# Kernel optimization log

Hardware: AMD Instinct MI355X
Metric: run time of the kernel (lower is better)

Reference implementation:

```python
import jax, jax.numpy as jnp
import numpy as np

DECAY = 0.99
EPS = 1e-05


def setup_inputs() -> dict:
    key = jax.random.key(0)
    k1, k2, k3 = jax.random.split(key, 3)
    x = jax.random.normal(k1, (16, 4096, 512), dtype=jnp.float32)
    embed = jax.random.normal(k2, (1024, 512), dtype=jnp.float32)
    cluster_size = jnp.ones((1024,), dtype=jnp.float32)
    embed_avg = jax.random.normal(k3, (1024, 512), dtype=jnp.float32)
    return {"x": x, "embed": embed, "cluster_size": cluster_size, "embed_avg": embed_avg}


def reference(x, embed, cluster_size, embed_avg):
    # x: [..., d]; embed: [K, d]
    K, d = embed.shape
    xf = x.reshape(-1, d)  # [N, d]
    dist = -(jnp.sum(xf * xf, axis=1, keepdims=True)
             - 2.0 * (xf @ embed.T)
             + jnp.sum(embed * embed, axis=1)[None, :])  # [N, K]
    ind = jnp.argmax(dist, axis=-1)  # [N]
    quantize = embed[ind].reshape(x.shape)  # dequantize (embedding lookup)
    embed_ind = ind.reshape(x.shape[:-1])
    # Training-mode EMA updates (one-hot scatter expressed as segment adds)
    counts = jnp.zeros((K,), dtype=x.dtype).at[ind].add(1.0)           # onehot.sum(0)
    embed_sum = jnp.zeros((K, d), dtype=x.dtype).at[ind].add(xf)       # (x^T @ onehot)^T
    new_cluster_size = cluster_size * DECAY + (1.0 - DECAY) * counts
    new_embed_avg = embed_avg * DECAY + (1.0 - DECAY) * embed_sum
    n = jnp.sum(new_cluster_size)
    cs = (new_cluster_size + EPS) / (n + K * EPS) * n  # laplace smoothing * total
    new_embed = new_embed_avg / cs[:, None]
    return (quantize, embed_ind, new_cluster_size, new_embed_avg, new_embed)
```

## Files before the change

kernel.cpp:

```cpp
#include <hip/hip_runtime.h>

typedef unsigned short ushort_t;
typedef __attribute__((ext_vector_type(8))) short bf16x8;
typedef __attribute__((ext_vector_type(4))) float f32x4;

#define DECAY 0.99f
#define EPS 1e-5f
#define K_CODES 1024
#define D 512
#define N_ROWS 65536
#define MARGIN 0.0625f

#define BM 128
#define NKT 8
#define NCH 16

#define CHUNK 64
#define MAX_CHUNKS 2048

#define XH_OFF   0u
#define XL_OFF   67108864u
#define EH_OFF   134217728u
#define EL_OFF   135266304u
#define ESUM_OFF 136314880u
#define CNT_OFF  138412032u
#define E2_OFF   138416128u
#define NFLAG_OFF 138420224u
#define NPTR_OFF  138420228u
#define FLAGS_OFF 138420480u
#define WS_NEED  (138420480u + 262144u)
#define ROWLIST_OFF   0u
#define BASE_OFF      262144u
#define CURSOR_OFF    266240u
#define CHUNKBASE_OFF 270336u
#define DESC_OFF      274432u
#define PARTIAL_OFF   307200u

__device__ inline ushort_t f2bf(float f) {
    unsigned int u = __float_as_uint(f);
    unsigned int r = (u + 0x7FFFu + ((u >> 16) & 1u)) >> 16;
    return (ushort_t)r;
}
__device__ inline float bf2f(ushort_t h) { return __uint_as_float(((unsigned int)h) << 16); }

__device__ inline void gload16_lds(const void* g, void* l) {
    __builtin_amdgcn_global_load_lds(
        (const __attribute__((address_space(1))) unsigned int*)g,
        (__attribute__((address_space(3))) unsigned int*)l, 16, 0, 0);
}

__global__ __launch_bounds__(256) void prep_split(const float* __restrict__ src,
                                                  ushort_t* __restrict__ hi,
                                                  ushort_t* __restrict__ lo) {
    const int g = blockIdx.x * 256 + threadIdx.x;
    const int ln = g & 63;
    const int tc = g >> 6;
    const int C = tc & 15;
    const int R = tc >> 4;
    const int row = (R << 4) + (ln & 15);
    const int k = (C << 5) + ((ln >> 4) << 3);
    const float4 v0 = *(const float4*)(src + (size_t)row * D + k);
    const float4 v1 = *(const float4*)(src + (size_t)row * D + k + 4);
    float v[8] = {v0.x, v0.y, v0.z, v0.w, v1.x, v1.y, v1.z, v1.w};
    short h[8], l[8];
    #pragma unroll
    for (int i = 0; i < 8; ++i) {
        ushort_t hh = f2bf(v[i]);
        h[i] = (short)hh;
        l[i] = (short)f2bf(v[i] - bf2f(hh));
    }
    bf16x8 hv = {h[0], h[1], h[2], h[3], h[4], h[5], h[6], h[7]};
    bf16x8 lv = {l[0], l[1], l[2], l[3], l[4], l[5], l[6], l[7]};
    *(bf16x8*)(hi + (size_t)g * 8) = hv;
    *(bf16x8*)(lo + (size_t)g * 8) = lv;
}

__global__ __launch_bounds__(64) void e2_kernel(const float* __restrict__ embed,
                                                float* __restrict__ e2) {
    const int k = blockIdx.x;
    const int t = threadIdx.x;
    const float* row = embed + (size_t)k * D;
    float s = 0.f;
    #pragma unroll
    for (int i = 0; i < D / 64; ++i) {
        float v = row[t + 64 * i];
        s = fmaf(v, v, s);
    }
    #pragma unroll
    for (int off = 32; off; off >>= 1) s += __shfl_down(s, off, 64);
    if (t == 0) e2[k] = s;
}

__global__ __launch_bounds__(256, 2) void vq_main(const ushort_t* __restrict__ xh,
                                                  const ushort_t* __restrict__ xl,
                                                  const ushort_t* __restrict__ eh,
                                                  const ushort_t* __restrict__ el,
                                                  const float* __restrict__ embed,
                                                  const float* __restrict__ e2,
                                                  float* __restrict__ out_q,
                                                  float* __restrict__ out_ind,
                                                  float* __restrict__ counts,
                                                  int* __restrict__ nflag,
                                                  int* __restrict__ flags) {
    __shared__ short sAh[4096], sAl[4096], sBh[4096], sBl[4096];
    __shared__ float se2[1024];
    __shared__ float red_b[128][2], red_s[128][2];
    __shared__ int   red_i[128][2];
    __shared__ int   bestk[128];

    const int tid = threadIdx.x;
    const int lane = tid & 63;
    const int w = tid >> 6;
    const int wm = w & 1;
    const int wn = w >> 1;
    const int R0 = blockIdx.x * 8;
    const int row0 = blockIdx.x * BM;

    for (int i = tid; i < 1024; i += 256) se2[i] = e2[i];

    const int ltile = lane << 3;

    float tb[16], ts[16];
    int ti[16];
    #pragma unroll
    for (int s = 0; s < 16; ++s) { tb[s] = -3.4e38f; ts[s] = -3.4e38f; ti[s] = 0; }

    for (int kt = 0; kt < NKT; ++kt) {
        f32x4 acc[4][4];
        #pragma unroll
        for (int mt = 0; mt < 4; ++mt)
            #pragma unroll
            for (int nt = 0; nt < 4; ++nt) acc[mt][nt] = (f32x4){0.f, 0.f, 0.f, 0.f};

        for (int c = 0; c < NCH; ++c) {
            __syncthreads();
            if (w == 0) {
                #pragma unroll
                for (int t = 0; t < 8; ++t)
                    gload16_lds(xh + ((size_t)((R0 + t) * 16 + c) << 9) + ltile, sAh + (t << 9));
            } else if (w == 1) {
                #pragma unroll
                for (int t = 0; t < 8; ++t)
                    gload16_lds(xl + ((size_t)((R0 + t) * 16 + c) << 9) + ltile, sAl + (t << 9));
            } else if (w == 2) {
                #pragma unroll
                for (int t = 0; t < 8; ++t)
                    gload16_lds(eh + ((size_t)(((kt << 3) + t) * 16 + c) << 9) + ltile, sBh + (t << 9));
            } else {
                #pragma unroll
                for (int t = 0; t < 8; ++t)
                    gload16_lds(el + ((size_t)(((kt << 3) + t) * 16 + c) << 9) + ltile, sBl + (t << 9));
            }
            __syncthreads();

            bf16x8 ah[4], al4[4], bh[4], bl[4];
            #pragma unroll
            for (int i = 0; i < 4; ++i) {
                ah[i]  = *(const bf16x8*)(sAh + (((wm << 2) + i) << 9) + ltile);
                al4[i] = *(const bf16x8*)(sAl + (((wm << 2) + i) << 9) + ltile);
                bh[i]  = *(const bf16x8*)(sBh + (((wn << 2) + i) << 9) + ltile);
                bl[i]  = *(const bf16x8*)(sBl + (((wn << 2) + i) << 9) + ltile);
            }
            #pragma unroll
            for (int nt = 0; nt < 4; ++nt) {
                #pragma unroll
                for (int mt = 0; mt < 4; ++mt) {
                    acc[mt][nt] = __builtin_amdgcn_mfma_f32_16x16x32_bf16(ah[mt], bh[nt], acc[mt][nt], 0, 0, 0);
                    acc[mt][nt] = __builtin_amdgcn_mfma_f32_16x16x32_bf16(al4[mt], bh[nt], acc[mt][nt], 0, 0, 0);
                    acc[mt][nt] = __builtin_amdgcn_mfma_f32_16x16x32_bf16(ah[mt], bl[nt], acc[mt][nt], 0, 0, 0);
                }
            }
        }

        #pragma unroll
        for (int nt = 0; nt < 4; ++nt) {
            const int code = (kt << 7) + (wn << 6) + (nt << 4) + (lane & 15);
            const float h = se2[code];
            #pragma unroll
            for (int mt = 0; mt < 4; ++mt) {
                #pragma unroll
                for (int r = 0; r < 4; ++r) {
                    const float v = fmaf(-0.5f, h, acc[mt][nt][r]);
                    const int s = (mt << 2) + r;
                    if (v > tb[s]) { ts[s] = tb[s]; tb[s] = v; ti[s] = code; }
                    else if (v > ts[s]) ts[s] = v;
                }
            }
        }
    }

    #pragma unroll
    for (int m = 1; m <= 8; m <<= 1) {
        #pragma unroll
        for (int s = 0; s < 16; ++s) {
            const float ob = __shfl_xor(tb[s], m, 64);
            const float os = __shfl_xor(ts[s], m, 64);
            const int oi = __shfl_xor(ti[s], m, 64);
            if (ob > tb[s] || (ob == tb[s] && oi < ti[s])) {
                ts[s] = fmaxf(tb[s], os); tb[s] = ob; ti[s] = oi;
            } else {
                ts[s] = fmaxf(ts[s], ob);
            }
        }
    }
    if ((lane & 15) == 0) {
        const int q = lane >> 4;
        #pragma unroll
        for (int mt = 0; mt < 4; ++mt)
            #pragma unroll
            for (int r = 0; r < 4; ++r) {
                const int rl = wm * 64 + mt * 16 + q * 4 + r;
                const int s = (mt << 2) + r;
                red_b[rl][wn] = tb[s]; red_s[rl][wn] = ts[s]; red_i[rl][wn] = ti[s];
            }
    }
    __syncthreads();

    if (tid < BM) {
        float b0 = red_b[tid][0], b1 = red_b[tid][1];
        float s0 = red_s[tid][0], s1 = red_s[tid][1];
        int i0 = red_i[tid][0], i1 = red_i[tid][1];
        float b, sec; int bi;
        if (b0 > b1 || (b0 == b1 && i0 < i1)) { b = b0; bi = i0; sec = fmaxf(s0, b1); }
        else { b = b1; bi = i1; sec = fmaxf(s1, b0); }
        bestk[tid] = bi;
        out_ind[row0 + tid] = (float)bi;
        atomicAdd(counts + bi, 1.0f);
        if (b - sec < MARGIN) {
            const int p = atomicAdd(nflag, 1);
            flags[p] = row0 + tid;
        }
    }
    __syncthreads();

    {
        const int f4 = tid & 127;
        const int rodd = tid >> 7;
        for (int it = 0; it < 64; ++it) {
            const int r = 2 * it + rodd;
            const int bk = bestk[r];
            const float4 q = ((const float4*)(embed + (size_t)bk * D))[f4];
            ((float4*)(out_q + (size_t)(row0 + r) * D))[f4] = q;
        }
    }
}

__global__ __launch_bounds__(256) void fixup(const float* __restrict__ x,
                                             const float* __restrict__ embed,
                                             const float* __restrict__ e2,
                                             const int* __restrict__ nflag,
                                             const int* __restrict__ flags,
                                             float* __restrict__ out_ind,
                                             float* __restrict__ out_q,
                                             float* __restrict__ counts) {
    __shared__ float xs[D];
    __shared__ float rb[256];
    __shared__ int ri[256];
    __shared__ int s_new;
    const int tid = threadIdx.x;
    const int n = *nflag;
    for (int fi = blockIdx.x; fi < n; fi += gridDim.x) {
        const int row = flags[fi];
        if (tid < 128) ((float4*)xs)[tid] = ((const float4*)(x + (size_t)row * D))[tid];
        __syncthreads();
        float best = -3.4e38f; int bi = 0;
        #pragma unroll
        for (int j = 0; j < 4; ++j) {
            const int c = tid * 4 + j;
            float acc = 0.f;
            const float4* ep = (const float4*)(embed + (size_t)c * D);
            for (int i4 = 0; i4 < 128; ++i4) {
                const float4 ev = ep[i4];
                const float4 xv = ((const float4*)xs)[i4];
                acc = fmaf(ev.x, xv.x, acc);
                acc = fmaf(ev.y, xv.y, acc);
                acc = fmaf(ev.z, xv.z, acc);
                acc = fmaf(ev.w, xv.w, acc);
            }
            const float sc = fmaf(-0.5f, e2[c], acc);
            if (sc > best) { best = sc; bi = c; }
        }
        rb[tid] = best; ri[tid] = bi;
        __syncthreads();
        for (int off = 128; off; off >>= 1) {
            if (tid < off) {
                if (rb[tid + off] > rb[tid] ||
                    (rb[tid + off] == rb[tid] && ri[tid + off] < ri[tid])) {
                    rb[tid] = rb[tid + off]; ri[tid] = ri[tid + off];
                }
            }
            __syncthreads();
        }
        if (tid == 0) {
            const int newi = ri[0];
            const int oldi = (int)out_ind[row];
            s_new = (newi == oldi) ? -1 : newi;
            if (newi != oldi) {
                out_ind[row] = (float)newi;
                atomicAdd(counts + oldi, -1.0f);
                atomicAdd(counts + newi, 1.0f);
            }
        }
        __syncthreads();
        const int nw = s_new;
        if (nw >= 0 && tid < 128) {
            const float4 q = ((const float4*)(embed + (size_t)nw * D))[tid];
            ((float4*)(out_q + (size_t)row * D))[tid] = q;
        }
        __syncthreads();
    }
}

__global__ __launch_bounds__(1024) void scan_kernel(const float* __restrict__ counts,
                                                    int* __restrict__ base,
                                                    int* __restrict__ cursor,
                                                    int* __restrict__ chunk_base,
                                                    int4* __restrict__ desc) {
    __shared__ int s[1024];
    const int t = threadIdx.x;
    const int c = (int)counts[t];
    s[t] = c;
    __syncthreads();
    #pragma unroll
    for (int off = 1; off < 1024; off <<= 1) {
        const int v = (t >= off) ? s[t - off] : 0;
        __syncthreads();
        s[t] += v;
        __syncthreads();
    }
    const int b = s[t] - c;
    base[t] = b;
    cursor[t] = b;
    const int nch = (c + CHUNK - 1) / CHUNK;
    s[t] = nch;
    __syncthreads();
    #pragma unroll
    for (int off = 1; off < 1024; off <<= 1) {
        const int v = (t >= off) ? s[t - off] : 0;
        __syncthreads();
        s[t] += v;
        __syncthreads();
    }
    const int cb = s[t] - nch;
    chunk_base[t] = cb;
    if (t == 1023) chunk_base[1024] = s[t];
    for (int j = 0; j < nch; ++j) {
        const int start = b + j * CHUNK;
        const int len = min(CHUNK, c - j * CHUNK);
        desc[cb + j] = make_int4(t, start, len, 0);
    }
}

__global__ __launch_bounds__(256) void scatter_kernel(const float* __restrict__ out_ind,
                                                      int* __restrict__ cursor,
                                                      int* __restrict__ rowlist) {
    const int g = blockIdx.x * 256 + threadIdx.x;
    const int code = (int)out_ind[g];
    const int pos = atomicAdd(cursor + code, 1);
    rowlist[pos] = g;
}

__global__ __launch_bounds__(128) void esum_partial(const float* __restrict__ x,
                                                    const int* __restrict__ chunk_base,
                                                    const int4* __restrict__ desc,
                                                    const int* __restrict__ rowlist,
                                                    float* __restrict__ partial) {
    const int b = blockIdx.x;
    if (b >= chunk_base[1024]) return;
    const int t = threadIdx.x;
    const int4 d = desc[b];
    const int b0 = d.y;
    const int cnt = d.z;
    float4 a0 = {0.f, 0.f, 0.f, 0.f}, a1 = {0.f, 0.f, 0.f, 0.f};
    float4 a2 = {0.f, 0.f, 0.f, 0.f}, a3 = {0.f, 0.f, 0.f, 0.f};
    int i = 0;
    for (; i + 4 <= cnt; i += 4) {
        const int r0 = rowlist[b0 + i];
        const int r1 = rowlist[b0 + i + 1];
        const int r2 = rowlist[b0 + i + 2];
        const int r3 = rowlist[b0 + i + 3];
        const float4 v0 = ((const float4*)x)[(size_t)r0 * 128 + t];
        const float4 v1 = ((const float4*)x)[(size_t)r1 * 128 + t];
        const float4 v2 = ((const float4*)x)[(size_t)r2 * 128 + t];
        const float4 v3 = ((const float4*)x)[(size_t)r3 * 128 + t];
        a0.x += v0.x; a0.y += v0.y; a0.z += v0.z; a0.w += v0.w;
        a1.x += v1.x; a1.y += v1.y; a1.z += v1.z; a1.w += v1.w;
        a2.x += v2.x; a2.y += v2.y; a2.z += v2.z; a2.w += v2.w;
        a3.x += v3.x; a3.y += v3.y; a3.z += v3.z; a3.w += v3.w;
    }
    for (; i < cnt; ++i) {
        const int r = rowlist[b0 + i];
        const float4 v = ((const float4*)x)[(size_t)r * 128 + t];
        a0.x += v.x; a0.y += v.y; a0.z += v.z; a0.w += v.w;
    }
    float4 s;
    s.x = (a0.x + a1.x) + (a2.x + a3.x);
    s.y = (a0.y + a1.y) + (a2.y + a3.y);
    s.z = (a0.z + a1.z) + (a2.z + a3.z);
    s.w = (a0.w + a1.w) + (a2.w + a3.w);
    ((float4*)partial)[(size_t)b * 128 + t] = s;
}

__global__ __launch_bounds__(128) void esum_final(const int* __restrict__ chunk_base,
                                                  const float* __restrict__ partial,
                                                  float* __restrict__ embed_sum) {
    const int k = blockIdx.x;
    const int t = threadIdx.x;
    const int c0 = chunk_base[k];
    const int c1 = chunk_base[k + 1];
    float4 a = {0.f, 0.f, 0.f, 0.f};
    for (int c = c0; c < c1; ++c) {
        const float4 v = ((const float4*)partial)[(size_t)c * 128 + t];
        a.x += v.x; a.y += v.y; a.z += v.z; a.w += v.w;
    }
    ((float4*)embed_sum)[(size_t)k * 128 + t] = a;
}

__global__ __launch_bounds__(256) void ema_cs(const float* __restrict__ cs,
                                              const float* __restrict__ counts,
                                              float* __restrict__ out_cs,
                                              float* __restrict__ nout) {
    __shared__ float red[256];
    const int t = threadIdx.x;
    const float4 c4 = ((const float4*)counts)[t];
    const float4 s4 = ((const float4*)cs)[t];
    float4 nc;
    nc.x = s4.x * DECAY + (1.f - DECAY) * c4.x;
    nc.y = s4.y * DECAY + (1.f - DECAY) * c4.y;
    nc.z = s4.z * DECAY + (1.f - DECAY) * c4.z;
    nc.w = s4.w * DECAY + (1.f - DECAY) * c4.w;
    ((float4*)out_cs)[t] = nc;
    red[t] = nc.x + nc.y + nc.z + nc.w;
    __syncthreads();
    #pragma unroll
    for (int off = 128; off; off >>= 1) {
        if (t < off) red[t] += red[t + off];
        __syncthreads();
    }
    if (t == 0) nout[0] = red[0];
}

__global__ __launch_bounds__(256) void ema_embed(const float* __restrict__ eavg,
                                                 const float* __restrict__ esum,
                                                 const float* __restrict__ ncs,
                                                 const float* __restrict__ nptr,
                                                 float* __restrict__ out_avg,
                                                 float* __restrict__ out_embed) {
    const int i4 = blockIdx.x * 256 + threadIdx.x;
    const int k = i4 >> 7;
    const float n = *nptr;
    const float csk = (ncs[k] + EPS) / (n + (float)K_CODES * EPS) * n;
    const float inv = 1.f / csk;
    const float4 a = ((const float4*)eavg)[i4];
    const float4 s = ((const float4*)esum)[i4];
    float4 na;
    na.x = a.x * DECAY + (1.f - DECAY) * s.x;
    na.y = a.y * DECAY + (1.f - DECAY) * s.y;
    na.z = a.z * DECAY + (1.f - DECAY) * s.z;
    na.w = a.w * DECAY + (1.f - DECAY) * s.w;
    ((float4*)out_avg)[i4] = na;
    float4 ne;
    ne.x = na.x * inv; ne.y = na.y * inv; ne.z = na.z * inv; ne.w = na.w * inv;
    ((float4*)out_embed)[i4] = ne;
}

#define MT2 128
#define S_STRIDE 132
__global__ __launch_bounds__(256, 2) void vq_main_f32(const float* __restrict__ x,
                                                      const float* __restrict__ embed,
                                                      const float* __restrict__ e2,
                                                      float* __restrict__ out_q,
                                                      float* __restrict__ out_ind,
                                                      float* __restrict__ counts,
                                                      float* __restrict__ embed_sum) {
    __shared__ float xs[32][S_STRIDE];
    __shared__ float es[32][S_STRIDE];
    __shared__ float rsc[MT2][17];
    __shared__ int rid[MT2][17];
    __shared__ int bestk[MT2];
    const int tid = threadIdx.x;
    const int lane = tid & 63;
    const int w = tid >> 6;
    const int tyg = (w & 1) * 8 + (lane >> 3);
    const int txg = (w >> 1) * 8 + (lane & 7);
    const int r0 = 8 * tyg, c0 = 8 * txg;
    const int row0 = blockIdx.x * MT2;
    const int sr = tid >> 3, sq = tid & 7;
    float best_s[8]; int best_i[8];
    #pragma unroll
    for (int r = 0; r < 8; ++r) { best_s[r] = -3.4e38f; best_i[r] = 0; }
    float4 px[4], pe[4];
    #pragma unroll
    for (int i = 0; i < 4; ++i) {
        px[i] = *(const float4*)(x + (size_t)(row0 + sr + 32 * i) * D + sq * 4);
        pe[i] = *(const float4*)(embed + (size_t)(sr + 32 * i) * D + sq * 4);
    }
    for (int kt = 0; kt < 8; ++kt) {
        const int k0 = kt * 128;
        float acc[8][8];
        #pragma unroll
        for (int j = 0; j < 8; ++j) {
            const float he = -0.5f * e2[k0 + c0 + j];
            #pragma unroll
            for (int r = 0; r < 8; ++r) acc[r][j] = he;
        }
        for (int dt = 0; dt < 16; ++dt) {
            __syncthreads();
            #pragma unroll
            for (int i = 0; i < 4; ++i) {
                const int rr = sr + 32 * i;
                #pragma unroll
                for (int ii = 0; ii < 4; ++ii) {
                    xs[sq * 4 + ii][rr] = ((const float*)&px[i])[ii];
                    es[sq * 4 + ii][rr] = ((const float*)&pe[i])[ii];
                }
            }
            __syncthreads();
            {
                const int s2 = kt * 16 + dt + 1;
                int kt2 = s2 >> 4; if (kt2 > 7) kt2 = 7;
                const int dt2 = s2 & 15;
                const int dof = dt2 * 32 + sq * 4;
                #pragma unroll
                for (int i = 0; i < 4; ++i) {
                    px[i] = *(const float4*)(x + (size_t)(row0 + sr + 32 * i) * D + dof);
                    pe[i] = *(const float4*)(embed + (size_t)(kt2 * 128 + sr + 32 * i) * D + dof);
                }
            }
            #pragma unroll 4
            for (int d = 0; d < 32; ++d) {
                const float4 xa = *(const float4*)&xs[d][r0];
                const float4 xb = *(const float4*)&xs[d][r0 + 4];
                const float4 ea = *(const float4*)&es[d][c0];
                const float4 eb = *(const float4*)&es[d][c0 + 4];
                const float xv[8] = {xa.x, xa.y, xa.z, xa.w, xb.x, xb.y, xb.z, xb.w};
                const float evv[8] = {ea.x, ea.y, ea.z, ea.w, eb.x, eb.y, eb.z, eb.w};
                #pragma unroll
                for (int r = 0; r < 8; ++r)
                    #pragma unroll
                    for (int j = 0; j < 8; ++j)
                        acc[r][j] = fmaf(xv[r], evv[j], acc[r][j]);
            }
        }
        #pragma unroll
        for (int j = 0; j < 8; ++j) {
            const int k = k0 + c0 + j;
            #pragma unroll
            for (int r = 0; r < 8; ++r)
                if (acc[r][j] > best_s[r]) { best_s[r] = acc[r][j]; best_i[r] = k; }
        }
    }
    #pragma unroll
    for (int r = 0; r < 8; ++r) { rsc[r0 + r][txg] = best_s[r]; rid[r0 + r][txg] = best_i[r]; }
    __syncthreads();
    if (tid < MT2) {
        float bs = rsc[tid][0]; int bk = rid[tid][0];
        #pragma unroll
        for (int g = 1; g < 16; ++g) {
            const float s = rsc[tid][g]; const int kk = rid[tid][g];
            if (s > bs || (s == bs && kk < bk)) { bs = s; bk = kk; }
        }
        bestk[tid] = bk;
        out_ind[row0 + tid] = (float)bk;
        atomicAdd(counts + bk, 1.0f);
    }
    __syncthreads();
    {
        const int f4 = tid & 127, rodd = tid >> 7;
        for (int it = 0; it < 64; ++it) {
            const int r = 2 * it + rodd;
            const int bk = bestk[r];
            const float4 q = ((const float4*)(embed + (size_t)bk * D))[f4];
            ((float4*)(out_q + (size_t)(row0 + r) * D))[f4] = q;
            const float4 xv = ((const float4*)(x + (size_t)(row0 + r) * D))[f4];
            float* sdst = embed_sum + (size_t)bk * D + f4 * 4;
            atomicAdd(sdst + 0, xv.x);
            atomicAdd(sdst + 1, xv.y);
            atomicAdd(sdst + 2, xv.z);
            atomicAdd(sdst + 3, xv.w);
        }
    }
}

extern "C" void kernel_launch(void* const* d_in, const int* in_sizes, int n_in,
                              void* d_out, int out_size, void* d_ws, size_t ws_size,
                              hipStream_t stream) {
    const float* x     = (const float*)d_in[0];
    const float* embed = (const float*)d_in[1];
    const float* cs    = (const float*)d_in[2];
    const float* eavg  = (const float*)d_in[3];

    float* out = (float*)d_out;
    float* out_q   = out;
    float* out_ind = out_q + (size_t)N_ROWS * D;
    float* out_cs  = out_ind + N_ROWS;
    float* out_avg = out_cs + K_CODES;
    float* out_emb = out_avg + (size_t)K_CODES * D;

    unsigned char* w = (unsigned char*)d_ws;

    if (ws_size >= WS_NEED) {
        ushort_t* xh = (ushort_t*)(w + XH_OFF);
        ushort_t* xl = (ushort_t*)(w + XL_OFF);
        ushort_t* eh = (ushort_t*)(w + EH_OFF);
        ushort_t* el = (ushort_t*)(w + EL_OFF);
        float* esum  = (float*)(w + ESUM_OFF);
        float* counts = (float*)(w + CNT_OFF);
        float* e2    = (float*)(w + E2_OFF);
        int* nflag   = (int*)(w + NFLAG_OFF);
        float* nptr  = (float*)(w + NPTR_OFF);
        int* flags   = (int*)(w + FLAGS_OFF);
        int* rowlist    = (int*)(w + ROWLIST_OFF);
        int* base       = (int*)(w + BASE_OFF);
        int* cursor     = (int*)(w + CURSOR_OFF);
        int* chunk_base = (int*)(w + CHUNKBASE_OFF);
        int4* desc      = (int4*)(w + DESC_OFF);
        float* partial  = (float*)(w + PARTIAL_OFF);

        hipMemsetAsync(counts, 0, 4096, stream);
        hipMemsetAsync(nflag, 0, 4, stream);
        prep_split<<<16384, 256, 0, stream>>>(x, xh, xl);
        prep_split<<<256, 256, 0, stream>>>(embed, eh, el);
        e2_kernel<<<K_CODES, 64, 0, stream>>>(embed, e2);
        vq_main<<<N_ROWS / BM, 256, 0, stream>>>(xh, xl, eh, el, embed, e2,
                                                 out_q, out_ind, counts, nflag, flags);
        fixup<<<1024, 256, 0, stream>>>(x, embed, e2, nflag, flags,
                                        out_ind, out_q, counts);
        scan_kernel<<<1, 1024, 0, stream>>>(counts, base, cursor, chunk_base, desc);
        scatter_kernel<<<N_ROWS / 256, 256, 0, stream>>>(out_ind, cursor, rowlist);
        esum_partial<<<MAX_CHUNKS, 128, 0, stream>>>(x, chunk_base, desc, rowlist, partial);
        esum_final<<<K_CODES, 128, 0, stream>>>(chunk_base, partial, esum);
        ema_cs<<<1, 256, 0, stream>>>(cs, counts, out_cs, nptr);
        ema_embed<<<(K_CODES * D / 4) / 256, 256, 0, stream>>>(eavg, esum, out_cs, nptr,
                                                               out_avg, out_emb);
    } else {
        float* counts = (float*)w;
        float* esum = counts + K_CODES;
        float* e2 = esum + (size_t)K_CODES * D;
        float* nptr = e2 + K_CODES;
        hipMemsetAsync(counts, 0, (size_t)(K_CODES + K_CODES * D) * sizeof(float), stream);
        e2_kernel<<<K_CODES, 64, 0, stream>>>(embed, e2);
        vq_main_f32<<<N_ROWS / MT2, 256, 0, stream>>>(x, embed, e2, out_q, out_ind, counts, esum);
        ema_cs<<<1, 256, 0, stream>>>(cs, counts, out_cs, nptr);
        ema_embed<<<(K_CODES * D / 4) / 256, 256, 0, stream>>>(eavg, esum, out_cs, nptr,
                                                               out_avg, out_emb);
    }
}
```

Baseline: 744.0 us.

## Double-buffer LDS tiles in VQ distance GEMM and swizzle block order

Splits the LDS staging buffers for x and codebook hi/lo bf16 tiles into two halves. The next chunk's global-to-LDS loads are issued before the MFMAs on the current chunk, which cuts one of the two barriers per chunk and lets the memory traffic overlap with the matrix math. It also remaps blockIdx so consecutive blocks take rows spread across the grid, which changes cache and channel locality. The cost is doubled LDS for the staging tiles, which could limit occupancy.

```diff
diff --git a/kernel.cpp b/kernel.cpp
--- a/kernel.cpp
+++ b/kernel.cpp
@@ -102,7 +102,7 @@
                                                   float* __restrict__ counts,
                                                   int* __restrict__ nflag,
                                                   int* __restrict__ flags) {
-    __shared__ short sAh[4096], sAl[4096], sBh[4096], sBl[4096];
+    __shared__ short sAh[2][4096], sAl[2][4096], sBh[2][4096], sBl[2][4096];
     __shared__ float se2[1024];
     __shared__ float red_b[128][2], red_s[128][2];
     __shared__ int   red_i[128][2];
@@ -113,18 +113,47 @@
     const int w = tid >> 6;
     const int wm = w & 1;
     const int wn = w >> 1;
-    const int R0 = blockIdx.x * 8;
-    const int row0 = blockIdx.x * BM;
+    const int bid = ((int)blockIdx.x & 7) * 64 + ((int)blockIdx.x >> 3);
+    const int R0 = bid * 8;
+    const int row0 = bid * BM;
 
     for (int i = tid; i < 1024; i += 256) se2[i] = e2[i];
 
     const int ltile = lane << 3;
+
+    #define STAGE(nk, nc, B) do {                                                              \
+        if (w == 0) {                                                                          \
+            _Pragma("unroll")                                                                  \
+            for (int t = 0; t < 8; ++t)                                                        \
+                gload16_lds(xh + ((size_t)((R0 + t) * 16 + (nc)) << 9) + ltile,                \
+                            &sAh[(B)][t << 9]);                                                \
+        } else if (w == 1) {                                                                   \
+            _Pragma("unroll")                                                                  \
+            for (int t = 0; t < 8; ++t)                                                        \
+                gload16_lds(xl + ((size_t)((R0 + t) * 16 + (nc)) << 9) + ltile,                \
+                            &sAl[(B)][t << 9]);                                                \
+        } else if (w == 2) {                                                                   \
+            _Pragma("unroll")                                                                  \
+            for (int t = 0; t < 8; ++t)                                                        \
+                gload16_lds(eh + ((size_t)((((nk) << 3) + t) * 16 + (nc)) << 9) + ltile,       \
+                            &sBh[(B)][t << 9]);                                                \
+        } else {                                                                               \
+            _Pragma("unroll")                                                                  \
+            for (int t = 0; t < 8; ++t)                                                        \
+                gload16_lds(el + ((size_t)((((nk) << 3) + t) * 16 + (nc)) << 9) + ltile,       \
+                            &sBl[(B)][t << 9]);                                                \
+        }                                                                                      \
+    } while (0)
 
     float tb[16], ts[16];
     int ti[16];
     #pragma unroll
     for (int s = 0; s < 16; ++s) { tb[s] = -3.4e38f; ts[s] = -3.4e38f; ti[s] = 0; }
 
+    STAGE(0, 0, 0);
+    __syncthreads();
+    int cur = 0;
+
     for (int kt = 0; kt < NKT; ++kt) {
         f32x4 acc[4][4];
         #pragma unroll
@@ -133,33 +162,20 @@
             for (int nt = 0; nt < 4; ++nt) acc[mt][nt] = (f32x4){0.f, 0.f, 0.f, 0.f};
 
         for (int c = 0; c < NCH; ++c) {
-            __syncthreads();
-            if (w == 0) {
-                #pragma unroll
-                for (int t = 0; t < 8; ++t)
-                    gload16_lds(xh + ((size_t)((R0 + t) * 16 + c) << 9) + ltile, sAh + (t << 9));
-            } else if (w == 1) {
-                #pragma unroll
-                for (int t = 0; t < 8; ++t)
-                    gload16_lds(xl + ((size_t)((R0 + t) * 16 + c) << 9) + ltile, sAl + (t << 9));
-            } else if (w == 2) {
-                #pragma unroll
-                for (int t = 0; t < 8; ++t)
-                    gload16_lds(eh + ((size_t)(((kt << 3) + t) * 16 + c) << 9) + ltile, sBh + (t << 9));
-            } else {
-                #pragma unroll
-                for (int t = 0; t < 8; ++t)
-                    gload16_lds(el + ((size_t)(((kt << 3) + t) * 16 + c) << 9) + ltile, sBl + (t << 9));
-            }
-            __syncthreads();
+            const int nxt = cur ^ 1;
+            if (!(kt == NKT - 1 && c == NCH - 1)) {
+                const int nk = (c == NCH - 1) ? kt + 1 : kt;
+                const int nc = (c == NCH - 1) ? 0 : c + 1;
+                STAGE(nk, nc, nxt);
+            }
 
             bf16x8 ah[4], al4[4], bh[4], bl[4];
             #pragma unroll
             for (int i = 0; i < 4; ++i) {
-                ah[i]  = *(const bf16x8*)(sAh + (((wm << 2) + i) << 9) + ltile);
-                al4[i] = *(const bf16x8*)(sAl + (((wm << 2) + i) << 9) + ltile);
-                bh[i]  = *(const bf16x8*)(sBh + (((wn << 2) + i) << 9) + ltile);
-                bl[i]  = *(const bf16x8*)(sBl + (((wn << 2) + i) << 9) + ltile);
+                ah[i]  = *(const bf16x8*)(&sAh[cur][(((wm << 2) + i) << 9) + ltile]);
+                al4[i] = *(const bf16x8*)(&sAl[cur][(((wm << 2) + i) << 9) + ltile]);
+                bh[i]  = *(const bf16x8*)(&sBh[cur][(((wn << 2) + i) << 9) + ltile]);
+                bl[i]  = *(const bf16x8*)(&sBl[cur][(((wn << 2) + i) << 9) + ltile]);
             }
             #pragma unroll
             for (int nt = 0; nt < 4; ++nt) {
@@ -170,6 +186,8 @@
                     acc[mt][nt] = __builtin_amdgcn_mfma_f32_16x16x32_bf16(ah[mt], bl[nt], acc[mt][nt], 0, 0, 0);
                 }
             }
+            __syncthreads();
+            cur = nxt;
         }
 
         #pragma unroll
@@ -188,6 +206,7 @@
             }
         }
     }
+    #undef STAGE
 
     #pragma unroll
     for (int m = 1; m <= 8; m <<= 1) {
```

Result: no change. 755.9 us (+1.6%).
